# Optimization experiments

Hardware: AMD Instinct MI355X
Metric: run time of the kernel (lower is better)

## Reference

```python
import jax, jax.numpy as jnp
import numpy as np

B, S, D, H = 2, 2048, 256, 8
W_STD = 0.02


def setup_inputs() -> dict:
    key = jax.random.key(0)
    ks = jax.random.split(key, 6)
    x = jax.random.normal(ks[0], (B, S, D), jnp.float32)
    e = jax.random.normal(ks[1], (B, S, D), jnp.float32)
    p = jax.random.normal(ks[2], (B, S, D), jnp.float32)
    W_q = W_STD * jax.random.normal(ks[3], (D, D), jnp.float32)
    W_k = W_STD * jax.random.normal(ks[4], (D, D), jnp.float32)
    W_v = W_STD * jax.random.normal(ks[5], (D, D), jnp.float32)
    gamma = jnp.ones((H, 1, 1), jnp.float32)
    return {"x": x, "e": e, "p": p, "W_q": W_q, "W_k": W_k, "W_v": W_v, "gamma": gamma}


def reference(x, e, p, W_q, W_k, W_v, gamma):
    # use_ppe=True: Q = K = p (broadcast to every head), V = e; each head sees
    # the SAME d_embed-wide copy, so project once and broadcast over heads.
    Q = p @ W_q  # [B,S,D]
    K = p @ W_k  # [B,S,D]
    V = e @ W_v  # [B,S,D]
    # squared euclidean distance (torch.cdist(...,p=2)**2), shared across heads
    q2 = jnp.sum(Q * Q, axis=-1)  # [B,S]
    k2 = jnp.sum(K * K, axis=-1)  # [B,S]
    d2 = q2[:, :, None] + k2[:, None, :] - 2.0 * jnp.einsum('bsd,btd->bst', Q, K)
    d2 = jnp.maximum(d2, 0.0)  # [B,S,S]
    # rbf kernel, per-head gamma: krn = exp(-d2 / (-2*gamma + 1e-6))
    krn = -d2[:, None, :, :] / (-2.0 * gamma + 1e-6)  # [B,H,S,S]
    causal = jnp.tril(jnp.ones((S, S), dtype=bool))  # True where attending allowed
    krn = jnp.where(causal, krn, -jnp.inf)
    krn = jnp.exp(krn)  # masked entries -> exp(-inf) = 0
    # dropout layers run in eval mode (identity)
    out = jnp.einsum('bhst,btd->bhsd', krn, V)  # [B,H,S,D]
    return out
```

## Files before the change

kernel.cpp:

```cpp
#include <hip/hip_runtime.h>
#include <hip/hip_bf16.h>


#define BB   2
#define SS   2048
#define DD   256
#define HH   8
#define BSR  (BB*SS)
#define TSPLIT 4

typedef __bf16 bf16_t;
typedef __bf16 bf16x8 __attribute__((ext_vector_type(8)));
typedef float  f32x4  __attribute__((ext_vector_type(4)));

static __device__ __forceinline__ f32x4 mfma16(bf16x8 a, bf16x8 b, f32x4 c) {
    return __builtin_amdgcn_mfma_f32_16x16x32_bf16(a, b, c, 0, 0, 0);
}

__global__ __launch_bounds__(256) void att_wtrans(
    const float* __restrict__ Wq, const float* __restrict__ Wk,
    const float* __restrict__ Wv,
    bf16_t* __restrict__ WFq_h, bf16_t* __restrict__ WFq_l,
    bf16_t* __restrict__ WFk_h, bf16_t* __restrict__ WFk_l,
    bf16_t* __restrict__ WFv, float* __restrict__ q2, float* __restrict__ k2)
{
    __shared__ float tT[64][68];
    const int tid = threadIdx.x;
    if (blockIdx.x == 48) {
        for (int i = tid; i < BSR; i += 256) { q2[i] = 0.f; k2[i] = 0.f; }
        return;
    }
    const int mat = blockIdx.x >> 4;
    const int tl  = blockIdx.x & 15;
    const int tr  = (tl >> 2) * 64, tc = (tl & 3) * 64;
    const float* W = (mat == 0) ? Wq : ((mat == 1) ? Wk : Wv);

#pragma unroll
    for (int i = 0; i < 4; ++i) {
        const int fidx = i * 256 + tid;
        const int r  = fidx >> 4;
        const int c4 = fidx & 15;
        const float4 v = *(const float4*)(W + (size_t)(tr + r) * DD + tc + c4 * 4);
        tT[c4 * 4 + 0][r] = v.x; tT[c4 * 4 + 1][r] = v.y;
        tT[c4 * 4 + 2][r] = v.z; tT[c4 * 4 + 3][r] = v.w;
    }
    __syncthreads();

#pragma unroll
    for (int i = 0; i < 2; ++i) {
        const int uidx  = i * 256 + tid;
        const int chunk = uidx >> 6;
        const int kc_l  = chunk >> 2, c16 = chunk & 3;
        const int u = uidx & 63, m16 = u & 15, quad = u >> 4;
        const float* src = &tT[c16 * 16 + m16][kc_l * 32 + quad * 8];
        const float4 a = *(const float4*)src;
        const float4 bq = *(const float4*)(src + 4);
        const float f[8] = {a.x, a.y, a.z, a.w, bq.x, bq.y, bq.z, bq.w};
        bf16x8 hi, lo;
#pragma unroll
        for (int j = 0; j < 8; ++j) {
            const bf16_t h = (bf16_t)f[j];
            hi[j] = h; lo[j] = (bf16_t)(f[j] - (float)h);
        }
        const int g16 = (tc >> 4) + c16;
        const int kcg = (tr >> 5) + kc_l;
        const size_t off = ((size_t)(g16 * 8 + kcg)) * 512 + (size_t)u * 8;
        if (mat == 0)      { *(bf16x8*)(WFq_h + off) = hi; *(bf16x8*)(WFq_l + off) = lo; }
        else if (mat == 1) { *(bf16x8*)(WFk_h + off) = hi; *(bf16x8*)(WFk_l + off) = lo; }
        else               { *(bf16x8*)(WFv + off)  = hi; }
    }
}

__global__ __launch_bounds__(256, 3) void att_gemm_qkv(
    const float* __restrict__ p, const float* __restrict__ e,
    const bf16_t* __restrict__ WFq_h, const bf16_t* __restrict__ WFq_l,
    const bf16_t* __restrict__ WFk_h, const bf16_t* __restrict__ WFk_l,
    const bf16_t* __restrict__ WFv,
    bf16_t* __restrict__ QFh, bf16_t* __restrict__ QFl,
    bf16_t* __restrict__ KFh, bf16_t* __restrict__ KFl,
    bf16_t* __restrict__ VF, float* __restrict__ q2, float* __restrict__ k2)
{
    __shared__ float pL[16][264];
    __shared__ float eL[16][264];
    __shared__ float fQ[16][68];
    __shared__ float fK[16][68];
    __shared__ float fV[16][68];

    const int tid  = threadIdx.x;
    const int w    = tid >> 6;
    const int lane = tid & 63;
    const int m16  = lane & 15;
    const int quad = lane >> 4;
    const int xcd  = blockIdx.x & 7;
    const int jid  = blockIdx.x >> 3;
    const int nb   = jid >> 5;
    const int row0 = (xcd * 32 + (jid & 31)) * 16;

#pragma unroll
    for (int i = 0; i < 4; ++i) {
        const int fidx = i * 256 + tid;
        const int r  = fidx >> 6;
        const int c4 = fidx & 63;
        const float4 pv = *(const float4*)(p + (size_t)(row0 + r) * DD + c4 * 4);
        const float4 ev = *(const float4*)(e + (size_t)(row0 + r) * DD + c4 * 4);
        *(float4*)&pL[r][c4 * 4] = pv;
        *(float4*)&eL[r][c4 * 4] = ev;
    }
    __syncthreads();

    f32x4 aQ = f32x4{0.f, 0.f, 0.f, 0.f};
    f32x4 aK = f32x4{0.f, 0.f, 0.f, 0.f};
    f32x4 aV = f32x4{0.f, 0.f, 0.f, 0.f};

#pragma unroll 2
    for (int kc = 0; kc < 8; ++kc) {
        const float* ps = &pL[m16][kc * 32 + quad * 8];
        const float* es = &eL[m16][kc * 32 + quad * 8];
        const float4 p0 = *(const float4*)ps;
        const float4 p1 = *(const float4*)(ps + 4);
        const float4 e0 = *(const float4*)es;
        const float4 e1 = *(const float4*)(es + 4);
        const float pa[8] = {p0.x, p0.y, p0.z, p0.w, p1.x, p1.y, p1.z, p1.w};
        const float ea[8] = {e0.x, e0.y, e0.z, e0.w, e1.x, e1.y, e1.z, e1.w};
        bf16x8 aph, apl, aeb;
#pragma unroll
        for (int j = 0; j < 8; ++j) {
            const bf16_t h = (bf16_t)pa[j];
            aph[j] = h;
            apl[j] = (bf16_t)(pa[j] - (float)h);
            aeb[j] = (bf16_t)ea[j];
        }
        const size_t wo = ((size_t)((nb * 4 + w) * 8 + kc)) * 512 + (size_t)lane * 8;
        const bf16x8 bqh = *(const bf16x8*)(WFq_h + wo);
        const bf16x8 bql = *(const bf16x8*)(WFq_l + wo);
        const bf16x8 bkh = *(const bf16x8*)(WFk_h + wo);
        const bf16x8 bkl = *(const bf16x8*)(WFk_l + wo);
        const bf16x8 bv  = *(const bf16x8*)(WFv + wo);
        aQ = mfma16(aph, bqh, aQ);
        aQ = mfma16(apl, bqh, aQ);
        aQ = mfma16(aph, bql, aQ);
        aK = mfma16(aph, bkh, aK);
        aK = mfma16(apl, bkh, aK);
        aK = mfma16(aph, bkl, aK);
        aV = mfma16(aeb, bv, aV);
    }

#pragma unroll
    for (int r = 0; r < 4; ++r) {
        const int rl = quad * 4 + r;
        fQ[rl][w * 16 + m16] = aQ[r];
        fK[rl][w * 16 + m16] = aK[r];
        fV[rl][w * 16 + m16] = aV[r];
    }

#pragma unroll
    for (int r = 0; r < 4; ++r) {
        float vq = aQ[r] * aQ[r], vk = aK[r] * aK[r];
#pragma unroll
        for (int off = 8; off >= 1; off >>= 1) {
            vq += __shfl_xor(vq, off);
            vk += __shfl_xor(vk, off);
        }
        if (m16 == 0) {
            atomicAdd(q2 + row0 + quad * 4 + r, vq);
            atomicAdd(k2 + row0 + quad * 4 + r, vk);
        }
    }

    __syncthreads();

    const int b   = row0 >> 11;
    const int sl  = row0 & 2047;
    const int tt  = sl >> 6;
    const int st  = sl >> 5;
    const int w4  = (sl >> 4) & 3;
    const int mt  = (sl >> 4) & 1;
    const int kc2 = (sl >> 5) & 1;
    const int uh  = (sl >> 4) & 1;

    if (w < 2) {
        const int cl = w;
        const float* src = &fQ[m16][cl * 32 + quad * 8];
        const float4 a = *(const float4*)src;
        const float4 c = *(const float4*)(src + 4);
        const float f[8] = {a.x, a.y, a.z, a.w, c.x, c.y, c.z, c.w};
        bf16x8 hi, lo;
#pragma unroll
        for (int j = 0; j < 8; ++j) {
            const bf16_t h = (bf16_t)f[j];
            hi[j] = h; lo[j] = (bf16_t)(f[j] - (float)h);
        }
        const size_t off = ((size_t)(b * 64 + st)) * 8192
                         + (size_t)(mt * 8 + nb * 2 + cl) * 512 + (size_t)lane * 8;
        *(bf16x8*)(QFh + off) = hi; *(bf16x8*)(QFl + off) = lo;
    } else {
        const int cl = w - 2;
        const float* src = &fK[m16][cl * 32 + quad * 8];
        const float4 a = *(const float4*)src;
        const float4 c = *(const float4*)(src + 4);
        const float f[8] = {a.x, a.y, a.z, a.w, c.x, c.y, c.z, c.w};
        bf16x8 hi, lo;
#pragma unroll
        for (int j = 0; j < 8; ++j) {
            const bf16_t h = (bf16_t)f[j];
            hi[j] = h; lo[j] = (bf16_t)(f[j] - (float)h);
        }
        const size_t off = ((size_t)(b * 32 + tt)) * 16384
                         + (size_t)(w4 * 8 + nb * 2 + cl) * 512 + (size_t)lane * 8;
        *(bf16x8*)(KFh + off) = hi; *(bf16x8*)(KFl + off) = lo;
    }

    if (lane < 32) {
        const int nt  = w;
        const int u   = uh * 32 + lane;
        const int tl0 = (lane >> 4) * 8;
        bf16x8 vb;
#pragma unroll
        for (int j = 0; j < 8; ++j)
            vb[j] = (bf16_t)fV[tl0 + j][nt * 16 + (lane & 15)];
        const size_t off = ((size_t)(b * 32 + tt)) * 16384
                         + (size_t)(nb * 8 + kc2 * 4 + nt) * 512 + (size_t)u * 8;
        *(bf16x8*)(VF + off) = vb;
    }
}

__global__ __launch_bounds__(256, 1) void att_flash(
    const bf16_t* __restrict__ QFh, const bf16_t* __restrict__ QFl,
    const bf16_t* __restrict__ KFh, const bf16_t* __restrict__ KFl,
    const bf16_t* __restrict__ VF, const float* __restrict__ q2,
    const float* __restrict__ k2, const float* __restrict__ gamma,
    float* __restrict__ part, float* __restrict__ out)
{
    __shared__ bf16_t Pb[2][2][32][72];

    const int tid   = threadIdx.x;
    const int pair  = blockIdx.x >> 3;
    const int sub   = blockIdx.x & 7;
    const int split = sub >> 1;
    const int b     = sub & 1;
    const int wave  = tid >> 6;
    const int lane  = tid & 63;
    const int m16   = lane & 15;
    const int quad  = lane >> 4;

    float g[8];
#pragma unroll
    for (int h = 0; h < 8; ++h) g[h] = gamma[h];

    int q = 0;

    for (int half = 0; half < 2; ++half) {
        const int st = half ? (63 - pair) : pair;
        const int s0 = st * 32;

        bf16x8 aQh[2][8], aQl[2][8];
        const size_t qtile = ((size_t)(b * 64 + st)) * 8192 + (size_t)lane * 8;
#pragma unroll
        for (int mt = 0; mt < 2; ++mt)
#pragma unroll
            for (int kc = 0; kc < 8; ++kc) {
                const size_t base = qtile + (size_t)(mt * 8 + kc) * 512;
                aQh[mt][kc] = *(const bf16x8*)(QFh + base);
                aQl[mt][kc] = *(const bf16x8*)(QFl + base);
            }

        float q2r[2][4];
#pragma unroll
        for (int mt = 0; mt < 2; ++mt)
#pragma unroll
            for (int r = 0; r < 4; ++r)
                q2r[mt][r] = q2[b * SS + s0 + mt * 16 + quad * 4 + r];

        const int n_tiles = (s0 + 31) / 64 + 1;

        for (int h = 0; h < HH; ++h) {
            int rep = 0;
            while (g[rep] != g[h]) ++rep;
            if (rep != h) continue;
            const float cexp = 1.0f / (2.0f * g[h] - 1e-6f);

            f32x4 O[2][4];
#pragma unroll
            for (int mt = 0; mt < 2; ++mt)
#pragma unroll
                for (int nt = 0; nt < 4; ++nt)
                    O[mt][nt] = f32x4{0.f, 0.f, 0.f, 0.f};

            int ti = split;

            while (ti + TSPLIT < n_tiles) {
                const int tiA = ti, tiB = ti + TSPLIT;
                const int tgA = tiA * 64 + wave * 16 + m16;
                const int tgB = tiB * 64 + wave * 16 + m16;
                const size_t tileA = ((size_t)(b * 32 + tiA)) * 16384
                                   + (size_t)wave * 4096 + (size_t)lane * 8;
                const size_t tileB = ((size_t)(b * 32 + tiB)) * 16384
                                   + (size_t)wave * 4096 + (size_t)lane * 8;

                bf16x8 vfA[2][4], vfB[2][4];
#pragma unroll
                for (int kc2 = 0; kc2 < 2; ++kc2)
#pragma unroll
                    for (int nt = 0; nt < 4; ++nt) {
                        vfA[kc2][nt] = *(const bf16x8*)(
                            VF + tileA + (size_t)(kc2 * 4 + nt) * 512);
                        vfB[kc2][nt] = *(const bf16x8*)(
                            VF + tileB + (size_t)(kc2 * 4 + nt) * 512);
                    }
                const float k2A = k2[b * SS + tgA];
                const float k2B = k2[b * SS + tgB];

                f32x4 aA0 = f32x4{0.f, 0.f, 0.f, 0.f};
                f32x4 aA1 = f32x4{0.f, 0.f, 0.f, 0.f};
                f32x4 aB0 = f32x4{0.f, 0.f, 0.f, 0.f};
                f32x4 aB1 = f32x4{0.f, 0.f, 0.f, 0.f};
#pragma unroll
                for (int kc = 0; kc < 8; ++kc) {
                    const bf16x8 bhA = *(const bf16x8*)(KFh + tileA + (size_t)kc * 512);
                    const bf16x8 blA = *(const bf16x8*)(KFl + tileA + (size_t)kc * 512);
                    const bf16x8 bhB = *(const bf16x8*)(KFh + tileB + (size_t)kc * 512);
                    const bf16x8 blB = *(const bf16x8*)(KFl + tileB + (size_t)kc * 512);
                    aA0 = mfma16(aQh[0][kc], bhA, aA0);
                    aA1 = mfma16(aQh[1][kc], bhA, aA1);
                    aB0 = mfma16(aQh[0][kc], bhB, aB0);
                    aB1 = mfma16(aQh[1][kc], bhB, aB1);
                    aA0 = mfma16(aQl[0][kc], bhA, aA0);
                    aA1 = mfma16(aQl[1][kc], bhA, aA1);
                    aB0 = mfma16(aQl[0][kc], bhB, aB0);
                    aB1 = mfma16(aQl[1][kc], bhB, aB1);
                    aA0 = mfma16(aQh[0][kc], blA, aA0);
                    aA1 = mfma16(aQh[1][kc], blA, aA1);
                    aB0 = mfma16(aQh[0][kc], blB, aB0);
                    aB1 = mfma16(aQh[1][kc], blB, aB1);
                }

#pragma unroll
                for (int mt = 0; mt < 2; ++mt) {
#pragma unroll
                    for (int r = 0; r < 4; ++r) {
                        const int sl = mt * 16 + quad * 4 + r;
                        const int sg = s0 + sl;
                        float dA = q2r[mt][r] + k2A
                                 - 2.0f * (mt ? aA1[r] : aA0[r]);
                        dA = fmaxf(dA, 0.0f);
                        const float wA = (tgA <= sg) ? __expf(cexp * dA) : 0.0f;
                        Pb[q][0][sl][wave * 16 + m16] = (bf16_t)wA;
                        float dB = q2r[mt][r] + k2B
                                 - 2.0f * (mt ? aB1[r] : aB0[r]);
                        dB = fmaxf(dB, 0.0f);
                        const float wB = (tgB <= sg) ? __expf(cexp * dB) : 0.0f;
                        Pb[q][1][sl][wave * 16 + m16] = (bf16_t)wB;
                    }
                }
                __syncthreads();

#pragma unroll
                for (int kc2 = 0; kc2 < 2; ++kc2) {
                    const bf16x8 pa0 = *(const bf16x8*)&Pb[q][0][m16][kc2 * 32 + quad * 8];
                    const bf16x8 pa1 = *(const bf16x8*)&Pb[q][0][m16 + 16][kc2 * 32 + quad * 8];
#pragma unroll
                    for (int nt = 0; nt < 4; ++nt) {
                        O[0][nt] = mfma16(pa0, vfA[kc2][nt], O[0][nt]);
                        O[1][nt] = mfma16(pa1, vfA[kc2][nt], O[1][nt]);
                    }
                }
#pragma unroll
                for (int kc2 = 0; kc2 < 2; ++kc2) {
                    const bf16x8 pb0 = *(const bf16x8*)&Pb[q][1][m16][kc2 * 32 + quad * 8];
                    const bf16x8 pb1 = *(const bf16x8*)&Pb[q][1][m16 + 16][kc2 * 32 + quad * 8];
#pragma unroll
                    for (int nt = 0; nt < 4; ++nt) {
                        O[0][nt] = mfma16(pb0, vfB[kc2][nt], O[0][nt]);
                        O[1][nt] = mfma16(pb1, vfB[kc2][nt], O[1][nt]);
                    }
                }
                q ^= 1;
                ti += 2 * TSPLIT;
            }

            if (ti < n_tiles) {
                const int tg = ti * 64 + wave * 16 + m16;
                const size_t tile = ((size_t)(b * 32 + ti)) * 16384
                                  + (size_t)wave * 4096 + (size_t)lane * 8;

                bf16x8 vf[2][4];
#pragma unroll
                for (int kc2 = 0; kc2 < 2; ++kc2)
#pragma unroll
                    for (int nt = 0; nt < 4; ++nt)
                        vf[kc2][nt] = *(const bf16x8*)(
                            VF + tile + (size_t)(kc2 * 4 + nt) * 512);
                const float k2v = k2[b * SS + tg];

                f32x4 acc0 = f32x4{0.f, 0.f, 0.f, 0.f};
                f32x4 acc1 = f32x4{0.f, 0.f, 0.f, 0.f};
#pragma unroll
                for (int kc = 0; kc < 8; ++kc) {
                    const bf16x8 bh = *(const bf16x8*)(KFh + tile + (size_t)kc * 512);
                    const bf16x8 bl = *(const bf16x8*)(KFl + tile + (size_t)kc * 512);
                    acc0 = mfma16(aQh[0][kc], bh, acc0);
                    acc1 = mfma16(aQh[1][kc], bh, acc1);
                    acc0 = mfma16(aQl[0][kc], bh, acc0);
                    acc1 = mfma16(aQl[1][kc], bh, acc1);
                    acc0 = mfma16(aQh[0][kc], bl, acc0);
                    acc1 = mfma16(aQh[1][kc], bl, acc1);
                }

#pragma unroll
                for (int mt = 0; mt < 2; ++mt) {
#pragma unroll
                    for (int r = 0; r < 4; ++r) {
                        const int sl = mt * 16 + quad * 4 + r;
                        const int sg = s0 + sl;
                        const float dotv = mt ? acc1[r] : acc0[r];
                        float d2 = q2r[mt][r] + k2v - 2.0f * dotv;
                        d2 = fmaxf(d2, 0.0f);
                        const float wgt = (tg <= sg) ? __expf(cexp * d2) : 0.0f;
                        Pb[q][0][sl][wave * 16 + m16] = (bf16_t)wgt;
                    }
                }
                __syncthreads();

#pragma unroll
                for (int kc2 = 0; kc2 < 2; ++kc2) {
                    const bf16x8 pa0 = *(const bf16x8*)&Pb[q][0][m16][kc2 * 32 + quad * 8];
                    const bf16x8 pa1 = *(const bf16x8*)&Pb[q][0][m16 + 16][kc2 * 32 + quad * 8];
#pragma unroll
                    for (int nt = 0; nt < 4; ++nt) {
                        O[0][nt] = mfma16(pa0, vf[kc2][nt], O[0][nt]);
                        O[1][nt] = mfma16(pa1, vf[kc2][nt], O[1][nt]);
                    }
                }
                q ^= 1;
            }

            float* dst = (split == 0)
                ? out  + (((size_t)b * HH + h) * SS + s0) * DD
                : part + ((((size_t)(split - 1) * BB + b) * HH + h) * SS + s0) * DD;
#pragma unroll
            for (int mt = 0; mt < 2; ++mt)
#pragma unroll
                for (int nt = 0; nt < 4; ++nt)
#pragma unroll
                    for (int r = 0; r < 4; ++r)
                        dst[(size_t)(mt * 16 + quad * 4 + r) * DD
                            + wave * 64 + nt * 16 + m16] = O[mt][nt][r];
        }
    }
}

__global__ __launch_bounds__(256) void att_reduce_bcast(
    const float* __restrict__ gamma, const float* __restrict__ part,
    float* __restrict__ out)
{
    const int j = blockIdx.x * 256 + threadIdx.x;
    const int b = blockIdx.y;
    const int slab = SS * DD / 4;

    float g[8];
#pragma unroll
    for (int h = 0; h < 8; ++h) g[h] = gamma[h];

    const float4* pp = (const float4*)part;
    float4* o4 = (float4*)out;

    float4 repval{0.f, 0.f, 0.f, 0.f};
    int last_rep = -1;
#pragma unroll
    for (int h = 0; h < HH; ++h) {
        int rep = 0;
        while (g[rep] != g[h]) ++rep;
        float4* o = o4 + ((size_t)(b * HH + h)) * slab + j;
        if (rep == h) {
            float4 v = *o;
#pragma unroll
            for (int k = 0; k < TSPLIT - 1; ++k) {
                const float4 pv = pp[(((size_t)k * BB + b) * HH + h) * slab + j];
                v.x += pv.x; v.y += pv.y; v.z += pv.z; v.w += pv.w;
            }
            *o = v; repval = v; last_rep = h;
        } else {
            if (last_rep != rep) {
                repval = o4[((size_t)(b * HH + rep)) * slab + j];
                last_rep = rep;
            }
            *o = repval;
        }
    }
}

extern "C" void kernel_launch(void* const* d_in, const int* in_sizes, int n_in,
                              void* d_out, int out_size, void* d_ws, size_t ws_size,
                              hipStream_t stream) {
    (void)in_sizes; (void)n_in; (void)out_size; (void)ws_size;
    const float* e     = (const float*)d_in[1];
    const float* p     = (const float*)d_in[2];
    const float* Wq    = (const float*)d_in[3];
    const float* Wk    = (const float*)d_in[4];
    const float* Wv    = (const float*)d_in[5];
    const float* gamma = (const float*)d_in[6];

    const size_t NROW = (size_t)BSR * DD;
    bf16_t* WFq_h = (bf16_t*)d_ws;
    bf16_t* WFq_l = WFq_h + DD * DD;
    bf16_t* WFk_h = WFq_l + DD * DD;
    bf16_t* WFk_l = WFk_h + DD * DD;
    bf16_t* WFv   = WFk_l + DD * DD;
    float*  q2    = (float*)(WFv + DD * DD);
    float*  k2    = q2 + BSR;
    bf16_t* QFh   = (bf16_t*)(k2 + BSR);
    bf16_t* QFl   = QFh + NROW;
    bf16_t* KFh   = QFl + NROW;
    bf16_t* KFl   = KFh + NROW;
    bf16_t* VF    = KFl + NROW;
    float*  part  = (float*)(VF + NROW);

    float* out = (float*)d_out;

    att_wtrans<<<dim3(49), dim3(256), 0, stream>>>(
        Wq, Wk, Wv, WFq_h, WFq_l, WFk_h, WFk_l, WFv, q2, k2);

    att_gemm_qkv<<<dim3((BSR / 16) * 4), dim3(256), 0, stream>>>(
        p, e, WFq_h, WFq_l, WFk_h, WFk_l, WFv, QFh, QFl, KFh, KFl, VF, q2, k2);

    att_flash<<<dim3(32 * TSPLIT * BB), dim3(256), 0, stream>>>(
        QFh, QFl, KFh, KFl, VF, q2, k2, gamma, part, out);

    att_reduce_bcast<<<dim3(SS * DD / 4 / 256, BB), dim3(256), 0, stream>>>(
        gamma, part, out);
}
```

Before: 128.0 us.

## Software-pipeline score computation with the previous tile's PV MFMAs

Restructures the causal tile loop so each iteration computes RBF scores for the next tile pair into one P buffer while running the P·V MFMAs on the pair written in the previous iteration. V fragments are loaded into a two-slot register array after the score step and consumed one iteration later, with a prologue and epilogue to handle dual and single tiles. The aim is to overlap the exp and LDS-store work with the PV matrix ops and hide V load latency, still with one barrier per iteration. The cost is more live registers (two V slots held across the score MFMAs), which could lower occupancy or cause spills.

New measurement: 127.0 us. Within noise of the previous version (-0.8%).

```diff
diff --git a/kernel.cpp b/kernel.cpp
--- a/kernel.cpp
+++ b/kernel.cpp
@@ -286,30 +286,17 @@
                 for (int nt = 0; nt < 4; ++nt)
                     O[mt][nt] = f32x4{0.f, 0.f, 0.f, 0.f};
 
-            int ti = split;
-
-            while (ti + TSPLIT < n_tiles) {
-                const int tiA = ti, tiB = ti + TSPLIT;
+            bf16x8 vf[2][2][4];
+
+            auto SCORES_DUAL = [&](int tiA, int tiB) {
                 const int tgA = tiA * 64 + wave * 16 + m16;
                 const int tgB = tiB * 64 + wave * 16 + m16;
                 const size_t tileA = ((size_t)(b * 32 + tiA)) * 16384
                                    + (size_t)wave * 4096 + (size_t)lane * 8;
                 const size_t tileB = ((size_t)(b * 32 + tiB)) * 16384
                                    + (size_t)wave * 4096 + (size_t)lane * 8;
-
-                bf16x8 vfA[2][4], vfB[2][4];
-#pragma unroll
-                for (int kc2 = 0; kc2 < 2; ++kc2)
-#pragma unroll
-                    for (int nt = 0; nt < 4; ++nt) {
-                        vfA[kc2][nt] = *(const bf16x8*)(
-                            VF + tileA + (size_t)(kc2 * 4 + nt) * 512);
-                        vfB[kc2][nt] = *(const bf16x8*)(
-                            VF + tileB + (size_t)(kc2 * 4 + nt) * 512);
-                    }
                 const float k2A = k2[b * SS + tgA];
                 const float k2B = k2[b * SS + tgB];
-
                 f32x4 aA0 = f32x4{0.f, 0.f, 0.f, 0.f};
                 f32x4 aA1 = f32x4{0.f, 0.f, 0.f, 0.f};
                 f32x4 aB0 = f32x4{0.f, 0.f, 0.f, 0.f};
@@ -333,65 +320,29 @@
                     aB0 = mfma16(aQh[0][kc], blB, aB0);
                     aB1 = mfma16(aQh[1][kc], blB, aB1);
                 }
-
 #pragma unroll
                 for (int mt = 0; mt < 2; ++mt) {
 #pragma unroll
                     for (int r = 0; r < 4; ++r) {
                         const int sl = mt * 16 + quad * 4 + r;
                         const int sg = s0 + sl;
-                        float dA = q2r[mt][r] + k2A
-                                 - 2.0f * (mt ? aA1[r] : aA0[r]);
+                        float dA = q2r[mt][r] + k2A - 2.0f * (mt ? aA1[r] : aA0[r]);
                         dA = fmaxf(dA, 0.0f);
-                        const float wA = (tgA <= sg) ? __expf(cexp * dA) : 0.0f;
-                        Pb[q][0][sl][wave * 16 + m16] = (bf16_t)wA;
-                        float dB = q2r[mt][r] + k2B
-                                 - 2.0f * (mt ? aB1[r] : aB0[r]);
+                        Pb[q][0][sl][wave * 16 + m16] =
+                            (bf16_t)((tgA <= sg) ? __expf(cexp * dA) : 0.0f);
+                        float dB = q2r[mt][r] + k2B - 2.0f * (mt ? aB1[r] : aB0[r]);
                         dB = fmaxf(dB, 0.0f);
-                        const float wB = (tgB <= sg) ? __expf(cexp * dB) : 0.0f;
-                        Pb[q][1][sl][wave * 16 + m16] = (bf16_t)wB;
+                        Pb[q][1][sl][wave * 16 + m16] =
+                            (bf16_t)((tgB <= sg) ? __expf(cexp * dB) : 0.0f);
                     }
                 }
-                __syncthreads();
-
-#pragma unroll
-                for (int kc2 = 0; kc2 < 2; ++kc2) {
-                    const bf16x8 pa0 = *(const bf16x8*)&Pb[q][0][m16][kc2 * 32 + quad * 8];
-                    const bf16x8 pa1 = *(const bf16x8*)&Pb[q][0][m16 + 16][kc2 * 32 + quad * 8];
-#pragma unroll
-                    for (int nt = 0; nt < 4; ++nt) {
-                        O[0][nt] = mfma16(pa0, vfA[kc2][nt], O[0][nt]);
-                        O[1][nt] = mfma16(pa1, vfA[kc2][nt], O[1][nt]);
-                    }
-                }
-#pragma unroll
-                for (int kc2 = 0; kc2 < 2; ++kc2) {
-                    const bf16x8 pb0 = *(const bf16x8*)&Pb[q][1][m16][kc2 * 32 + quad * 8];
-                    const bf16x8 pb1 = *(const bf16x8*)&Pb[q][1][m16 + 16][kc2 * 32 + quad * 8];
-#pragma unroll
-                    for (int nt = 0; nt < 4; ++nt) {
-                        O[0][nt] = mfma16(pb0, vfB[kc2][nt], O[0][nt]);
-                        O[1][nt] = mfma16(pb1, vfB[kc2][nt], O[1][nt]);
-                    }
-                }
-                q ^= 1;
-                ti += 2 * TSPLIT;
-            }
-
-            if (ti < n_tiles) {
-                const int tg = ti * 64 + wave * 16 + m16;
-                const size_t tile = ((size_t)(b * 32 + ti)) * 16384
+            };
+
+            auto SCORES_SINGLE = [&](int tiA) {
+                const int tg = tiA * 64 + wave * 16 + m16;
+                const size_t tile = ((size_t)(b * 32 + tiA)) * 16384
                                   + (size_t)wave * 4096 + (size_t)lane * 8;
-
-                bf16x8 vf[2][4];
-#pragma unroll
-                for (int kc2 = 0; kc2 < 2; ++kc2)
-#pragma unroll
-                    for (int nt = 0; nt < 4; ++nt)
-                        vf[kc2][nt] = *(const bf16x8*)(
-                            VF + tile + (size_t)(kc2 * 4 + nt) * 512);
                 const float k2v = k2[b * SS + tg];
-
                 f32x4 acc0 = f32x4{0.f, 0.f, 0.f, 0.f};
                 f32x4 acc1 = f32x4{0.f, 0.f, 0.f, 0.f};
 #pragma unroll
@@ -405,33 +356,84 @@
                     acc0 = mfma16(aQh[0][kc], bl, acc0);
                     acc1 = mfma16(aQh[1][kc], bl, acc1);
                 }
-
 #pragma unroll
                 for (int mt = 0; mt < 2; ++mt) {
 #pragma unroll
                     for (int r = 0; r < 4; ++r) {
                         const int sl = mt * 16 + quad * 4 + r;
                         const int sg = s0 + sl;
-                        const float dotv = mt ? acc1[r] : acc0[r];
-                        float d2 = q2r[mt][r] + k2v - 2.0f * dotv;
+                        float d2 = q2r[mt][r] + k2v - 2.0f * (mt ? acc1[r] : acc0[r]);
                         d2 = fmaxf(d2, 0.0f);
-                        const float wgt = (tg <= sg) ? __expf(cexp * d2) : 0.0f;
-                        Pb[q][0][sl][wave * 16 + m16] = (bf16_t)wgt;
+                        Pb[q][0][sl][wave * 16 + m16] =
+                            (bf16_t)((tg <= sg) ? __expf(cexp * d2) : 0.0f);
                     }
                 }
+            };
+
+            auto PV_ONE = [&](int slot) {
+#pragma unroll
+                for (int kc2 = 0; kc2 < 2; ++kc2) {
+                    const bf16x8 pa0 = *(const bf16x8*)
+                        &Pb[q ^ 1][slot][m16][kc2 * 32 + quad * 8];
+                    const bf16x8 pa1 = *(const bf16x8*)
+                        &Pb[q ^ 1][slot][m16 + 16][kc2 * 32 + quad * 8];
+#pragma unroll
+                    for (int nt = 0; nt < 4; ++nt) {
+                        O[0][nt] = mfma16(pa0, vf[slot][kc2][nt], O[0][nt]);
+                        O[1][nt] = mfma16(pa1, vf[slot][kc2][nt], O[1][nt]);
+                    }
+                }
+            };
+
+            auto LOADV = [&](int slot, int tiX) {
+                const size_t tile = ((size_t)(b * 32 + tiX)) * 16384
+                                  + (size_t)wave * 4096 + (size_t)lane * 8;
+#pragma unroll
+                for (int kc2 = 0; kc2 < 2; ++kc2)
+#pragma unroll
+                    for (int nt = 0; nt < 4; ++nt)
+                        vf[slot][kc2][nt] = *(const bf16x8*)(
+                            VF + tile + (size_t)(kc2 * 4 + nt) * 512);
+            };
+
+            int ti = split;
+            bool pendDual = false;
+
+            if (ti < n_tiles) {
+                const bool dual0 = (ti + TSPLIT < n_tiles);
+                if (dual0) {
+                    SCORES_DUAL(ti, ti + TSPLIT);
+                    LOADV(0, ti); LOADV(1, ti + TSPLIT);
+                } else {
+                    SCORES_SINGLE(ti);
+                    LOADV(0, ti);
+                }
                 __syncthreads();
-
-#pragma unroll
-                for (int kc2 = 0; kc2 < 2; ++kc2) {
-                    const bf16x8 pa0 = *(const bf16x8*)&Pb[q][0][m16][kc2 * 32 + quad * 8];
-                    const bf16x8 pa1 = *(const bf16x8*)&Pb[q][0][m16 + 16][kc2 * 32 + quad * 8];
-#pragma unroll
-                    for (int nt = 0; nt < 4; ++nt) {
-                        O[0][nt] = mfma16(pa0, vf[kc2][nt], O[0][nt]);
-                        O[1][nt] = mfma16(pa1, vf[kc2][nt], O[1][nt]);
-                    }
-                }
                 q ^= 1;
+                pendDual = dual0;
+                ti += dual0 ? 2 * TSPLIT : TSPLIT;
+
+                while (ti + TSPLIT < n_tiles) {
+                    SCORES_DUAL(ti, ti + TSPLIT);
+                    PV_ONE(0); PV_ONE(1);
+                    LOADV(0, ti); LOADV(1, ti + TSPLIT);
+                    __syncthreads();
+                    q ^= 1;
+                    ti += 2 * TSPLIT;
+                }
+
+                if (ti < n_tiles) {
+                    SCORES_SINGLE(ti);
+                    PV_ONE(0); PV_ONE(1);
+                    LOADV(0, ti);
+                    __syncthreads();
+                    q ^= 1;
+                    pendDual = false;
+                    ti += TSPLIT;
+                }
+
+                PV_ONE(0);
+                if (pendDual) PV_ONE(1);
             }
 
             float* dst = (split == 0)
```
